# Performance work log

Measured on AMD Instinct MI355X. Metric: run time of the kernel, lower is better.

Reference implementation:

```python
import jax, jax.numpy as jnp
import numpy as np

G, P = 512, 128            # graphs, nodes per graph
NT, NL, NC = 120, 4, 4     # tracks/leptons/cells per graph (disjoint node targets)
W_NODE, W_BCE, W_F1 = 1.0, 1.0, 1.0  # config['loss weights']


def setup_inputs() -> dict:
    key = jax.random.key(0)
    ks = jax.random.split(key, 8)
    N = G * P
    T, L, C = G * NT, G * NL, G * NC
    E = G * P * P
    local = np.arange(P)[None, :] + (np.arange(G)[:, None] * P)  # [G,P] global node ids
    track_dst = jnp.asarray(local[:, :NT].ravel(), jnp.int32)
    lep_dst = jnp.asarray(local[:, NT:NT + NL].ravel(), jnp.int32)
    cell_dst = jnp.asarray(local[:, NT + NL:].ravel(), jnp.int32)
    ii, jj = np.meshgrid(np.arange(P), np.arange(P), indexing='ij')
    off = (np.arange(G) * P)[:, None, None]
    edge_src = jnp.asarray((off + ii[None]).reshape(-1), jnp.int32)
    edge_dst = jnp.asarray((off + jj[None]).reshape(-1), jnp.int32)
    edge_gid = jnp.asarray(np.repeat(np.arange(G), P * P), jnp.int32)
    node_gid = jnp.asarray(np.repeat(np.arange(G), P), jnp.int32)
    return {
        'node_prediction': jax.random.normal(ks[0], (N, 5), jnp.float32),
        'edge_prediction': jax.random.normal(ks[1], (E,), jnp.float32),
        'ce_weight': jnp.ones((5,), jnp.float32),
        'track_labels': jax.random.randint(ks[2], (T,), 0, 5, jnp.int32),
        'track_vtx': jax.random.randint(ks[3], (T,), 0, 10, jnp.int32),
        'lep_labels': jax.random.randint(ks[4], (L,), 0, 5, jnp.int32),
        'lep_vtx': jax.random.randint(ks[5], (L,), 0, 10, jnp.int32),
        'cell_labels': jax.random.randint(ks[6], (C,), 0, 5, jnp.int32),
        'cell_vtx': jax.random.randint(ks[7], (C,), 0, 10, jnp.int32),
        'track_dst': track_dst,
        'lep_dst': lep_dst,
        'cell_dst': cell_dst,
        'edge_src': edge_src,
        'edge_dst': edge_dst,
        'edge_gid': edge_gid,
        'node_gid': node_gid,
    }


def reference(node_prediction, edge_prediction, ce_weight,
              track_labels, track_vtx, lep_labels, lep_vtx, cell_labels, cell_vtx,
              track_dst, lep_dst, cell_dst, edge_src, edge_dst, edge_gid, node_gid):
    N = node_prediction.shape[0]

    def scatter(track_v, lep_v, cell_v):  # copy_src + sum over 3 edge types
        out = jnp.zeros((N,), jnp.int32)
        out = out.at[track_dst].add(track_v)
        out = out.at[lep_dst].add(lep_v)
        out = out.at[cell_dst].add(cell_v)
        return out

    node_labels = scatter(track_labels, lep_labels, cell_labels)
    node_vtx = scatter(track_vtx, lep_vtx, cell_vtx)

    # node CrossEntropyLoss (weight=[1]*5, ignore_index=-1, reduction='none')
    logp = jax.nn.log_softmax(node_prediction, axis=-1)
    valid = node_labels != -1
    lab = jnp.clip(node_labels, 0, 4)
    ce = -jnp.take_along_axis(logp, lab[:, None], axis=-1)[:, 0] * ce_weight[lab]
    ce = jnp.where(valid, ce, 0.0)
    node_loss = jax.ops.segment_sum(ce, node_gid, num_segments=G).mean()

    # edge weights (EdgeWeightFunction) and labels (EdgeLabelFunction)
    src_lab = node_labels[edge_src]
    dst_lab = node_labels[edge_dst]
    cond = ((dst_lab == 3) | (dst_lab == 2)) & ((src_lab == 3) | (src_lab == 2))
    w = jnp.where(cond, 2.0, 1.0).astype(jnp.float32)
    y = (node_vtx[edge_src] == node_vtx[edge_dst]).astype(jnp.float32)

    x = edge_prediction
    # BCEWithLogits: log(1+e^x) - x*y
    bce = (jnp.logaddexp(0.0, x) - x * y) * w
    e_cnt = jax.ops.segment_sum(jnp.ones_like(x), edge_gid, num_segments=G)
    edge_bce = (jax.ops.segment_sum(bce, edge_gid, num_segments=G) / e_cnt).mean()

    yh = jax.nn.sigmoid(x)
    tp = jax.ops.segment_sum(yh * y * w, edge_gid, num_segments=G)
    fn = jax.ops.segment_sum((1.0 - yh) * y * w, edge_gid, num_segments=G)
    fp = jax.ops.segment_sum(yh * (1.0 - y) * w, edge_gid, num_segments=G)
    edge_f1 = -(2.0 * tp / (2.0 * tp + fp + fn + 1e-10)).mean()

    loss = node_loss * W_NODE + edge_bce * W_BCE + edge_f1 * W_F1
    return loss
```

## Files before the change

### kernel.cpp

```cpp
#include <hip/hip_runtime.h>
#include <math.h>

#define NG     512
#define NP     128
#define NTRK   120
#define NLEP   4
#define NCEL   4
#define EPG    (NP * NP)
#define NTHREADS 256
#define SPLIT  4
#define EPB    (EPG / SPLIT)
#define F4ITERS (EPB / (NTHREADS * 4))

__global__ __launch_bounds__(NTHREADS) void vfl_main(
    const float* __restrict__ node_pred,
    const float* __restrict__ edge_pred,
    const float* __restrict__ ce_weight,
    const int* __restrict__ track_labels, const int* __restrict__ track_vtx,
    const int* __restrict__ lep_labels,   const int* __restrict__ lep_vtx,
    const int* __restrict__ cell_labels,  const int* __restrict__ cell_vtx,
    float* __restrict__ gout)
{
    const int b = blockIdx.x;
    const int g = b >> 2;
    const int s = b & 3;
    const int t = threadIdx.x;

    __shared__ int   s_pack[NP];
    __shared__ float s_red[4][5];
    __shared__ int   s_cnt[10][2];

    if (t < 20) ((int*)s_cnt)[t] = 0;

    float ce = 0.0f;
    int vtx = 0, is23 = 0;
    if (t < NP) {
        int lab;
        if (t < NTRK) {
            lab = track_labels[g * NTRK + t];
            vtx = track_vtx  [g * NTRK + t];
        } else if (t < NTRK + NLEP) {
            const int u = t - NTRK;
            lab = lep_labels[g * NLEP + u];
            vtx = lep_vtx  [g * NLEP + u];
        } else {
            const int u = t - NTRK - NLEP;
            lab = cell_labels[g * NCEL + u];
            vtx = cell_vtx  [g * NCEL + u];
        }
        is23 = (lab == 2 || lab == 3) ? 1 : 0;
        s_pack[t] = (vtx & 0xff) | (is23 << 8);

        if (s == 0) {
            const float* np = node_pred + (size_t)(g * NP + t) * 5;
            const float x0 = np[0], x1 = np[1], x2 = np[2], x3 = np[3], x4 = np[4];
            const float m  = fmaxf(fmaxf(fmaxf(x0, x1), fmaxf(x2, x3)), x4);
            const float sm = __expf(x0 - m) + __expf(x1 - m) + __expf(x2 - m)
                           + __expf(x3 - m) + __expf(x4 - m);
            const float lse = m + __logf(sm);
            const float xl = (lab == 0) ? x0 : (lab == 1) ? x1 : (lab == 2) ? x2
                           : (lab == 3) ? x3 : x4;
            ce = (lse - xl) * ce_weight[lab];
        }
    }
    __syncthreads();

    if (s == 0 && t < NP) atomicAdd(&s_cnt[vtx][is23], 1);

    const int j0 = (t & 31) << 2;
    const int pj0 = s_pack[j0 + 0];
    const int pj1 = s_pack[j0 + 1];
    const int pj2 = s_pack[j0 + 2];
    const int pj3 = s_pack[j0 + 3];
    const int ibase = s * 32 + (t >> 5);

    const float4* ep4 = (const float4*)(edge_pred + (size_t)g * EPG + (size_t)s * EPB);

    float bce = 0.0f, swyh = 0.0f, tp = 0.0f;

    #pragma unroll
    for (int k = 0; k < F4ITERS; ++k) {
        const float4 v  = ep4[k * NTHREADS + t];
        const int    pi = s_pack[ibase + k * 8];

        const float xs[4]  = { v.x, v.y, v.z, v.w };
        const int   pjs[4] = { pj0, pj1, pj2, pj3 };
        #pragma unroll
        for (int c = 0; c < 4; ++c) {
            const float x   = xs[c];
            const int   pjc = pjs[c];
            const bool  same = (((pi ^ pjc) & 0xff) == 0);
            const float w   = ((pi & pjc) & 0x100) ? 2.0f : 1.0f;
            const float wf  = same ? w : 0.0f;
            const float e  = __expf(-fabsf(x));
            const float t1 = 1.0f + e;
            const float r  = __builtin_amdgcn_rcpf(t1);
            const float sp = fmaxf(x, 0.0f) + __logf(t1);
            const float yh = (x >= 0.0f) ? r : (1.0f - r);
            bce  = fmaf(w,  sp, bce);
            bce  = fmaf(wf, -x, bce);
            swyh = fmaf(w,  yh, swyh);
            tp   = fmaf(wf, yh, tp);
        }
    }

    float vals[4] = { ce, bce, swyh, tp };
    #pragma unroll
    for (int i = 0; i < 4; ++i) {
        float x = vals[i];
        #pragma unroll
        for (int off = 32; off > 0; off >>= 1)
            x += __shfl_xor(x, off, 64);
        vals[i] = x;
    }
    const int wave = t >> 6;
    const int lane = t & 63;
    if (lane == 0) {
        #pragma unroll
        for (int i = 0; i < 4; ++i) s_red[wave][i] = vals[i];
    }
    __syncthreads();
    if (t == 0) {
        float* gp = gout + (size_t)b * 5;
        #pragma unroll
        for (int i = 0; i < 4; ++i)
            gp[i] = s_red[0][i] + s_red[1][i] + s_red[2][i] + s_red[3][i];
        int swfy = 0;
        if (s == 0) {
            #pragma unroll
            for (int v = 0; v < 10; ++v) {
                const int n0 = s_cnt[v][0], n1 = s_cnt[v][1];
                const int nt = n0 + n1;
                swfy += nt * nt + n1 * n1;
            }
        }
        gp[4] = (float)swfy;
    }
}

__global__ __launch_bounds__(256) void vfl_finalize(
    const float* __restrict__ gout, float* __restrict__ out)
{
    const int t = threadIdx.x;
    float ce = 0.0f, bce = 0.0f, f1 = 0.0f;
    for (int g = t; g < NG; g += 256) {
        const float* p = gout + (size_t)g * SPLIT * 5;
        float gce = 0.0f, gbce = 0.0f, gswyh = 0.0f, gtp = 0.0f, gswfy = 0.0f;
        #pragma unroll
        for (int s = 0; s < SPLIT; ++s) {
            gce   += p[s * 5 + 0];
            gbce  += p[s * 5 + 1];
            gswyh += p[s * 5 + 2];
            gtp   += p[s * 5 + 3];
            gswfy += p[s * 5 + 4];
        }
        ce  += gce;
        bce += gbce;
        const float fn = gswfy - gtp;
        const float fp = gswyh - gtp;
        f1  += (2.0f * gtp) / (2.0f * gtp + fp + fn + 1e-10f);
    }
    #pragma unroll
    for (int off = 32; off > 0; off >>= 1) {
        ce  += __shfl_xor(ce,  off, 64);
        bce += __shfl_xor(bce, off, 64);
        f1  += __shfl_xor(f1,  off, 64);
    }
    __shared__ float sred[4][3];
    const int wave = t >> 6;
    const int lane = t & 63;
    if (lane == 0) { sred[wave][0] = ce; sred[wave][1] = bce; sred[wave][2] = f1; }
    __syncthreads();
    if (t == 0) {
        const float tce  = sred[0][0] + sred[1][0] + sred[2][0] + sred[3][0];
        const float tbce = sred[0][1] + sred[1][1] + sred[2][1] + sred[3][1];
        const float tf1  = sred[0][2] + sred[1][2] + sred[2][2] + sred[3][2];
        out[0] = tce * (1.0f / NG)
               + tbce * (1.0f / ((float)NG * (float)EPG))
               - tf1 * (1.0f / NG);
    }
}

extern "C" void kernel_launch(void* const* d_in, const int* in_sizes, int n_in,
                              void* d_out, int out_size, void* d_ws, size_t ws_size,
                              hipStream_t stream)
{
    const float* node_pred    = (const float*)d_in[0];
    const float* edge_pred    = (const float*)d_in[1];
    const float* ce_weight    = (const float*)d_in[2];
    const int*   track_labels = (const int*)d_in[3];
    const int*   track_vtx    = (const int*)d_in[4];
    const int*   lep_labels   = (const int*)d_in[5];
    const int*   lep_vtx      = (const int*)d_in[6];
    const int*   cell_labels  = (const int*)d_in[7];
    const int*   cell_vtx     = (const int*)d_in[8];

    float* gout = (float*)d_ws;
    float* out  = (float*)d_out;

    vfl_main<<<NG * SPLIT, NTHREADS, 0, stream>>>(
        node_pred, edge_pred, ce_weight,
        track_labels, track_vtx, lep_labels, lep_vtx, cell_labels, cell_vtx,
        gout);
    vfl_finalize<<<1, 256, 0, stream>>>(gout, out);
}
```

Before: 18.87 us.

## Fuse finalize into main kernel via last-block atomic counter reduction

Merges the separate finalize kernel into the main kernel: each block publishes its partials, bumps a global atomic counter, and the last block to finish does the cross-graph reduction. It also spreads the per-graph node cross-entropy across the four split blocks instead of only the first, and stores partials in a structure-of-arrays layout. This removes one kernel launch and the gap between launches, in exchange for a threadfence plus atomic in every block and reliance on the counter being reset.

```diff
diff --git a/kernel.cpp b/kernel.cpp
--- a/kernel.cpp
+++ b/kernel.cpp
@@ -9,17 +9,21 @@
 #define EPG    (NP * NP)
 #define NTHREADS 256
 #define SPLIT  4
+#define NBLK   (NG * SPLIT)
 #define EPB    (EPG / SPLIT)
 #define F4ITERS (EPB / (NTHREADS * 4))
 
-__global__ __launch_bounds__(NTHREADS) void vfl_main(
+__device__ int g_done = 0;
+
+__global__ __launch_bounds__(NTHREADS, 4) void vfl_fused(
     const float* __restrict__ node_pred,
     const float* __restrict__ edge_pred,
     const float* __restrict__ ce_weight,
     const int* __restrict__ track_labels, const int* __restrict__ track_vtx,
     const int* __restrict__ lep_labels,   const int* __restrict__ lep_vtx,
     const int* __restrict__ cell_labels,  const int* __restrict__ cell_vtx,
-    float* __restrict__ gout)
+    float* __restrict__ gout,
+    float* __restrict__ out)
 {
     const int b = blockIdx.x;
     const int g = b >> 2;
@@ -27,8 +31,9 @@
     const int t = threadIdx.x;
 
     __shared__ int   s_pack[NP];
-    __shared__ float s_red[4][5];
+    __shared__ float s_red[4][4];
     __shared__ int   s_cnt[10][2];
+    __shared__ int   s_last;
 
     if (t < 20) ((int*)s_cnt)[t] = 0;
 
@@ -51,7 +56,7 @@
         is23 = (lab == 2 || lab == 3) ? 1 : 0;
         s_pack[t] = (vtx & 0xff) | (is23 << 8);
 
-        if (s == 0) {
+        if ((t >> 5) == s) {
             const float* np = node_pred + (size_t)(g * NP + t) * 5;
             const float x0 = np[0], x1 = np[1], x2 = np[2], x3 = np[3], x4 = np[4];
             const float m  = fmaxf(fmaxf(fmaxf(x0, x1), fmaxf(x2, x3)), x4);
@@ -120,61 +125,67 @@
         for (int i = 0; i < 4; ++i) s_red[wave][i] = vals[i];
     }
     __syncthreads();
+
     if (t == 0) {
-        float* gp = gout + (size_t)b * 5;
         #pragma unroll
         for (int i = 0; i < 4; ++i)
-            gp[i] = s_red[0][i] + s_red[1][i] + s_red[2][i] + s_red[3][i];
-        int swfy = 0;
+            gout[i * NBLK + b] = s_red[0][i] + s_red[1][i] + s_red[2][i] + s_red[3][i];
         if (s == 0) {
+            int swfy = 0;
             #pragma unroll
             for (int v = 0; v < 10; ++v) {
                 const int n0 = s_cnt[v][0], n1 = s_cnt[v][1];
                 const int nt = n0 + n1;
                 swfy += nt * nt + n1 * n1;
             }
-        }
-        gp[4] = (float)swfy;
-    }
-}
-
-__global__ __launch_bounds__(256) void vfl_finalize(
-    const float* __restrict__ gout, float* __restrict__ out)
-{
-    const int t = threadIdx.x;
-    float ce = 0.0f, bce = 0.0f, f1 = 0.0f;
-    for (int g = t; g < NG; g += 256) {
-        const float* p = gout + (size_t)g * SPLIT * 5;
-        float gce = 0.0f, gbce = 0.0f, gswyh = 0.0f, gtp = 0.0f, gswfy = 0.0f;
-        #pragma unroll
-        for (int s = 0; s < SPLIT; ++s) {
-            gce   += p[s * 5 + 0];
-            gbce  += p[s * 5 + 1];
-            gswyh += p[s * 5 + 2];
-            gtp   += p[s * 5 + 3];
-            gswfy += p[s * 5 + 4];
-        }
-        ce  += gce;
-        bce += gbce;
+            gout[4 * NBLK + b] = (float)swfy;
+        }
+        __threadfence();
+        const int old = atomicAdd(&g_done, 1);
+        if (old == NBLK - 1) {
+            g_done = 0;
+            s_last = 1;
+        } else {
+            s_last = 0;
+        }
+    }
+    __syncthreads();
+    if (!s_last) return;
+
+    __threadfence();
+
+    float fce = 0.0f, fbce = 0.0f, ff1 = 0.0f;
+    for (int g2 = t; g2 < NG; g2 += NTHREADS) {
+        float gce = 0.0f, gbce = 0.0f, gswyh = 0.0f, gtp = 0.0f;
+        #pragma unroll
+        for (int q = 0; q < SPLIT; ++q) {
+            const int idx = g2 * SPLIT + q;
+            gce   += gout[0 * NBLK + idx];
+            gbce  += gout[1 * NBLK + idx];
+            gswyh += gout[2 * NBLK + idx];
+            gtp   += gout[3 * NBLK + idx];
+        }
+        const float gswfy = gout[4 * NBLK + g2 * SPLIT];
+        fce  += gce;
+        fbce += gbce;
         const float fn = gswfy - gtp;
         const float fp = gswyh - gtp;
-        f1  += (2.0f * gtp) / (2.0f * gtp + fp + fn + 1e-10f);
+        ff1  += (2.0f * gtp) / (2.0f * gtp + fp + fn + 1e-10f);
     }
     #pragma unroll
     for (int off = 32; off > 0; off >>= 1) {
-        ce  += __shfl_xor(ce,  off, 64);
-        bce += __shfl_xor(bce, off, 64);
-        f1  += __shfl_xor(f1,  off, 64);
-    }
-    __shared__ float sred[4][3];
-    const int wave = t >> 6;
-    const int lane = t & 63;
-    if (lane == 0) { sred[wave][0] = ce; sred[wave][1] = bce; sred[wave][2] = f1; }
+        fce  += __shfl_xor(fce,  off, 64);
+        fbce += __shfl_xor(fbce, off, 64);
+        ff1  += __shfl_xor(ff1,  off, 64);
+    }
+    if (lane == 0) {
+        s_red[wave][0] = fce; s_red[wave][1] = fbce; s_red[wave][2] = ff1;
+    }
     __syncthreads();
     if (t == 0) {
-        const float tce  = sred[0][0] + sred[1][0] + sred[2][0] + sred[3][0];
-        const float tbce = sred[0][1] + sred[1][1] + sred[2][1] + sred[3][1];
-        const float tf1  = sred[0][2] + sred[1][2] + sred[2][2] + sred[3][2];
+        const float tce  = s_red[0][0] + s_red[1][0] + s_red[2][0] + s_red[3][0];
+        const float tbce = s_red[0][1] + s_red[1][1] + s_red[2][1] + s_red[3][1];
+        const float tf1  = s_red[0][2] + s_red[1][2] + s_red[2][2] + s_red[3][2];
         out[0] = tce * (1.0f / NG)
                + tbce * (1.0f / ((float)NG * (float)EPG))
                - tf1 * (1.0f / NG);
@@ -198,9 +209,8 @@
     float* gout = (float*)d_ws;
     float* out  = (float*)d_out;
 
-    vfl_main<<<NG * SPLIT, NTHREADS, 0, stream>>>(
+    vfl_fused<<<NBLK, NTHREADS, 0, stream>>>(
         node_pred, edge_pred, ce_weight,
         track_labels, track_vtx, lep_labels, lep_vtx, cell_labels, cell_vtx,
-        gout);
-    vfl_finalize<<<1, 256, 0, stream>>>(gout, out);
+        gout, out);
 }
```

Measured after the change: 65.45 us. +246.8%, slower.

## Stage edge predictions into LDS via async global_load_lds and spread CE work

Applied to the files above, without the earlier changes.

Each block issues direct global-to-LDS loads for its 16 KB slice of edge logits at kernel start, so the transfer overlaps with label loading and the node cross-entropy. The compute loop then reads from LDS. The CE computation is spread across the four split blocks instead of all landing on split 0. The workspace moves to a struct-of-arrays layout for coalesced reads in finalize. This adds 16 KB of LDS per block, which may reduce occupancy.

```diff
diff --git a/kernel.cpp b/kernel.cpp
--- a/kernel.cpp
+++ b/kernel.cpp
@@ -9,8 +9,10 @@
 #define EPG    (NP * NP)
 #define NTHREADS 256
 #define SPLIT  4
+#define NBLK   (NG * SPLIT)
 #define EPB    (EPG / SPLIT)
 #define F4ITERS (EPB / (NTHREADS * 4))
+
 
 __global__ __launch_bounds__(NTHREADS) void vfl_main(
     const float* __restrict__ node_pred,
@@ -26,9 +28,25 @@
     const int s = b & 3;
     const int t = threadIdx.x;
 
+    __shared__ float s_edge[EPB];
     __shared__ int   s_pack[NP];
-    __shared__ float s_red[4][5];
+    __shared__ float s_red[4][4];
     __shared__ int   s_cnt[10][2];
+
+    {
+        const float* ep_base = edge_pred + (size_t)g * EPG + (size_t)s * EPB;
+        const int wv = t >> 6;
+        const int ln = t & 63;
+        #pragma unroll
+        for (int k = 0; k < 4; ++k) {
+            const int c = (k << 2) + wv;
+            const float* gsrc = ep_base + c * 256 + ln * 4;
+            __builtin_amdgcn_global_load_lds(
+                (const __attribute__((address_space(1))) void*)gsrc,
+                (__attribute__((address_space(3))) void*)&s_edge[c * 256],
+                16, 0, 0);
+        }
+    }
 
     if (t < 20) ((int*)s_cnt)[t] = 0;
 
@@ -51,7 +69,7 @@
         is23 = (lab == 2 || lab == 3) ? 1 : 0;
         s_pack[t] = (vtx & 0xff) | (is23 << 8);
 
-        if (s == 0) {
+        if ((t >> 5) == s) {
             const float* np = node_pred + (size_t)(g * NP + t) * 5;
             const float x0 = np[0], x1 = np[1], x2 = np[2], x3 = np[3], x4 = np[4];
             const float m  = fmaxf(fmaxf(fmaxf(x0, x1), fmaxf(x2, x3)), x4);
@@ -63,6 +81,8 @@
             ce = (lse - xl) * ce_weight[lab];
         }
     }
+
+    asm volatile("s_waitcnt vmcnt(0)" ::: "memory");
     __syncthreads();
 
     if (s == 0 && t < NP) atomicAdd(&s_cnt[vtx][is23], 1);
@@ -74,13 +94,13 @@
     const int pj3 = s_pack[j0 + 3];
     const int ibase = s * 32 + (t >> 5);
 
-    const float4* ep4 = (const float4*)(edge_pred + (size_t)g * EPG + (size_t)s * EPB);
+    const float4* se4 = (const float4*)s_edge;
 
     float bce = 0.0f, swyh = 0.0f, tp = 0.0f;
 
     #pragma unroll
     for (int k = 0; k < F4ITERS; ++k) {
-        const float4 v  = ep4[k * NTHREADS + t];
+        const float4 v  = se4[k * NTHREADS + t];
         const int    pi = s_pack[ibase + k * 8];
 
         const float xs[4]  = { v.x, v.y, v.z, v.w };
@@ -120,21 +140,21 @@
         for (int i = 0; i < 4; ++i) s_red[wave][i] = vals[i];
     }
     __syncthreads();
+
     if (t == 0) {
-        float* gp = gout + (size_t)b * 5;
         #pragma unroll
         for (int i = 0; i < 4; ++i)
-            gp[i] = s_red[0][i] + s_red[1][i] + s_red[2][i] + s_red[3][i];
-        int swfy = 0;
+            gout[i * NBLK + b] = s_red[0][i] + s_red[1][i] + s_red[2][i] + s_red[3][i];
         if (s == 0) {
+            int swfy = 0;
             #pragma unroll
-            for (int v = 0; v < 10; ++v) {
-                const int n0 = s_cnt[v][0], n1 = s_cnt[v][1];
+            for (int vv = 0; vv < 10; ++vv) {
+                const int n0 = s_cnt[vv][0], n1 = s_cnt[vv][1];
                 const int nt = n0 + n1;
                 swfy += nt * nt + n1 * n1;
             }
-        }
-        gp[4] = (float)swfy;
+            gout[4 * NBLK + b] = (float)swfy;
+        }
     }
 }
 
@@ -143,17 +163,17 @@
 {
     const int t = threadIdx.x;
     float ce = 0.0f, bce = 0.0f, f1 = 0.0f;
-    for (int g = t; g < NG; g += 256) {
-        const float* p = gout + (size_t)g * SPLIT * 5;
-        float gce = 0.0f, gbce = 0.0f, gswyh = 0.0f, gtp = 0.0f, gswfy = 0.0f;
-        #pragma unroll
-        for (int s = 0; s < SPLIT; ++s) {
-            gce   += p[s * 5 + 0];
-            gbce  += p[s * 5 + 1];
-            gswyh += p[s * 5 + 2];
-            gtp   += p[s * 5 + 3];
-            gswfy += p[s * 5 + 4];
-        }
+    for (int g2 = t; g2 < NG; g2 += 256) {
+        float gce = 0.0f, gbce = 0.0f, gswyh = 0.0f, gtp = 0.0f;
+        #pragma unroll
+        for (int q = 0; q < SPLIT; ++q) {
+            const int idx = g2 * SPLIT + q;
+            gce   += gout[0 * NBLK + idx];
+            gbce  += gout[1 * NBLK + idx];
+            gswyh += gout[2 * NBLK + idx];
+            gtp   += gout[3 * NBLK + idx];
+        }
+        const float gswfy = gout[4 * NBLK + g2 * SPLIT];
         ce  += gce;
         bce += gbce;
         const float fn = gswfy - gtp;
@@ -198,7 +218,7 @@
     float* gout = (float*)d_ws;
     float* out  = (float*)d_out;
 
-    vfl_main<<<NG * SPLIT, NTHREADS, 0, stream>>>(
+    vfl_main<<<NBLK, NTHREADS, 0, stream>>>(
         node_pred, edge_pred, ce_weight,
         track_labels, track_vtx, lep_labels, lep_vtx, cell_labels, cell_vtx,
         gout);
```

After: 20.90 us. 10.7% more time.
